# Performance work log

Hardware: AMD Instinct MI355X
Metric: run time of the kernel (lower is better)

The kernel has to match this reference:

```python
import jax, jax.numpy as jnp
import numpy as np

# Hard-coded problem constants from WENONetwork.forward()
SIGMA = 0.3
RATE = 0.1
STRIKE = 50.0
T_FINAL = 1.0
XL, XR = -6.0, 1.5
M = 80                      # spatial cells -> M+1 nodes
H = (XR - XL) / M
# explicit-Euler diffusion CFL: dt = 0.4*h^2/sigma^2
N_STEPS = int(np.ceil(T_FINAL / (0.4 * H * H / SIGMA ** 2)))
DT = T_FINAL / N_STEPS
ADV = RATE - 0.5 * SIGMA ** 2   # drift in log-price variable


def setup_inputs() -> dict:
    key = jax.random.key(0)
    k5, k6 = jax.random.split(key)
    # learned WENO weights: convex combinations over 3 candidate stencils
    omegas5 = jax.nn.softmax(jax.random.normal(k5, (M, 3), dtype=jnp.float32), axis=-1)
    omegas6 = jax.nn.softmax(jax.random.normal(k6, (M - 1, 3), dtype=jnp.float32), axis=-1)
    return {"omegas5": omegas5, "omegas6": omegas6}


def _bs_weno(omegas5, omegas6):
    # log-price grid and terminal-payoff initial condition for a call
    x = jnp.linspace(XL, XR, M + 1)
    S = STRIKE * jnp.exp(x)
    u0 = jnp.maximum(S - STRIKE, 0.0).astype(jnp.float32)

    w5_0, w5_1, w5_2 = omegas5[:, 0], omegas5[:, 1], omegas5[:, 2]  # per-interface, [M]
    w6_0, w6_1, w6_2 = omegas6[:, 0], omegas6[:, 1], omegas6[:, 2]  # per interior node, [M-1]
    s_right = S[-1]

    def step(carry, _):
        u, t = carry
        # ghost cells: flat-extend left (payoff is 0 there), linear-extrapolate right
        left = jnp.full((2,), u[0], u.dtype)
        right = u[-1] + jnp.arange(1, 3, dtype=u.dtype) * (u[-1] - u[-2])
        up = jnp.concatenate([left, u, right])  # nodes -2 .. M+2, node k -> up[k+2]

        # ---- WENO5 left-biased reconstruction at interfaces j+1/2, j = 0..M-1 ----
        um2 = up[0:M]; um1 = up[1:M + 1]; uc = up[2:M + 2]
        up1 = up[3:M + 3]; up2 = up[4:M + 4]
        f0 = (2.0 * um2 - 7.0 * um1 + 11.0 * uc) / 6.0
        f1 = (-um1 + 5.0 * uc + 2.0 * up1) / 6.0
        f2 = (2.0 * uc + 5.0 * up1 - up2) / 6.0
        uhat = w5_0 * f0 + w5_1 * f1 + w5_2 * f2          # [M] interface values
        ux = (uhat[1:] - uhat[:-1]) / H                   # [M-1] first derivative at nodes 1..M-1

        # ---- WENO-weighted second derivative at interior nodes i = 1..M-1 ----
        dm2 = up[1:M]; dm1 = up[2:M + 1]; dc = up[3:M + 2]
        dp1 = up[4:M + 3]; dp2 = up[5:M + 4]
        c0 = dm2 - 2.0 * dm1 + dc
        c1 = dm1 - 2.0 * dc + dp1
        c2 = dc - 2.0 * dp1 + dp2
        uxx = (w6_0 * c0 + w6_1 * c1 + w6_2 * c2) / (H * H)  # [M-1]

        # explicit Euler update of Black-Scholes PDE in log variable
        du = 0.5 * SIGMA ** 2 * uxx + ADV * ux - RATE * u[1:M]
        tn = t + DT
        bc_right = (s_right - STRIKE * jnp.exp(-RATE * tn)).astype(u.dtype)
        un = jnp.concatenate([jnp.zeros((1,), u.dtype),
                              u[1:M] + DT * du,
                              bc_right[None]])
        return (un, tn), None

    (uT, _), _ = jax.lax.scan(step, (u0, jnp.float32(0.0)), None, length=N_STEPS)
    return uT


def reference(omegas5, omegas6):
    return _bs_weno(omegas5, omegas6)
```

## Files before the change

### kernel.cpp

```cpp
#include <hip/hip_runtime.h>
#include <hip/hip_bf16.h>


#define MM 80
#define NSTEPS 26

__global__ __launch_bounds__(128)
void weno_bs_kernel(const float* __restrict__ om5,
                    const float* __restrict__ om6,
                    float* __restrict__ out)
{
    const float H      = 7.5f / 80.0f;
    const float DT     = 1.0f / 26.0f;
    const float SIG2H2 = 0.045f / (H * H);
    const float ADV    = 0.055f;
    const float RATE   = 0.1f;
    const float STRIKE = 50.0f;

    __shared__ float up[MM + 5];
    __shared__ float uhat[MM];

    const int i = threadIdx.x;

    float w50 = 0.f, w51 = 0.f, w52 = 0.f;
    float w60 = 0.f, w61 = 0.f, w62 = 0.f;
    if (i < MM) {
        w50 = om5[3 * i + 0];
        w51 = om5[3 * i + 1];
        w52 = om5[3 * i + 2];
    }
    if (i >= 1 && i <= MM - 1) {
        const int j = i - 1;
        w60 = om6[3 * j + 0];
        w61 = om6[3 * j + 1];
        w62 = om6[3 * j + 2];
    }

    if (i <= MM) {
        float x = -6.0f + (float)i * H;
        float S = STRIKE * expf(x);
        up[2 + i] = fmaxf(S - STRIKE, 0.0f);
    }
    const float s_right = STRIKE * expf(1.5f);
    float t = 0.0f;
    __syncthreads();

    for (int step = 0; step < NSTEPS; ++step) {
        if (i == 0) {
            float u0v = up[2];
            up[0] = u0v;
            up[1] = u0v;
            float d = up[2 + MM] - up[1 + MM];
            up[3 + MM] = up[2 + MM] + d;
            up[4 + MM] = up[2 + MM] + 2.0f * d;
        }
        __syncthreads();

        float a0 = 0.f, a1 = 0.f, a2 = 0.f, a3 = 0.f, a4 = 0.f;
        float uxx = 0.f, uold = 0.f;
        if (i < MM) {
            a0 = up[i];     a1 = up[i + 1]; a2 = up[i + 2];
            a3 = up[i + 3]; a4 = up[i + 4];
            float f0 = (2.0f * a0 - 7.0f * a1 + 11.0f * a2) * (1.0f / 6.0f);
            float f1 = (-a1 + 5.0f * a2 + 2.0f * a3) * (1.0f / 6.0f);
            float f2 = (2.0f * a2 + 5.0f * a3 - a4) * (1.0f / 6.0f);
            uhat[i] = w50 * f0 + w51 * f1 + w52 * f2;
        }
        if (i >= 1 && i <= MM - 1) {
            float c0 = a0 - 2.0f * a1 + a2;
            float c1 = a1 - 2.0f * a2 + a3;
            float c2 = a2 - 2.0f * a3 + a4;
            uxx  = w60 * c0 + w61 * c1 + w62 * c2;
            uold = a2;
        }
        t += DT;
        __syncthreads();

        if (i >= 1 && i <= MM - 1) {
            float ux = (uhat[i] - uhat[i - 1]) / H;
            float du = SIG2H2 * uxx + ADV * ux - RATE * uold;
            up[2 + i] = uold + DT * du;
        } else if (i == 0) {
            up[2] = 0.0f;
        } else if (i == MM) {
            up[2 + MM] = s_right - STRIKE * expf(-RATE * t);
        }
        __syncthreads();
    }

    if (i <= MM) {
        out[i] = up[2 + i];
    }
}

extern "C" void kernel_launch(void* const* d_in, const int* in_sizes, int n_in,
                              void* d_out, int out_size, void* d_ws, size_t ws_size,
                              hipStream_t stream) {
    const float* om5 = (const float*)d_in[0];
    const float* om6 = (const float*)d_in[1];
    float* out = (float*)d_out;
    weno_bs_kernel<<<dim3(1), dim3(128), 0, stream>>>(om5, om6, out);
}
```

Before: 66.55 us.

## Run WENO stepper in a single wavefront with register shuffles instead of LDS barriers

Replaces the 128-thread block with one 64-lane wavefront in which each lane owns two grid nodes. Neighbour values are exchanged through warp shuffles rather than shared memory, which removes all __syncthreads barriers and LDS round-trips from the 26-step serial loop. The boundary discount factor is now updated by repeated multiplication instead of an exp per step, which may differ slightly in rounding from the reference. Correctness depends on the per-lane boundary handling for lanes 0, 39 and 40.

```diff
diff --git a/kernel.cpp b/kernel.cpp
--- a/kernel.cpp
+++ b/kernel.cpp
@@ -1,96 +1,80 @@
 #include <hip/hip_runtime.h>
-#include <hip/hip_bf16.h>
 
 
 #define MM 80
 #define NSTEPS 26
 
-__global__ __launch_bounds__(128)
+__global__ __launch_bounds__(64)
 void weno_bs_kernel(const float* __restrict__ om5,
                     const float* __restrict__ om6,
                     float* __restrict__ out)
 {
-    const float H      = 7.5f / 80.0f;
+    const float H      = 0.09375f;
+    const float INV_H  = 1.0f / 0.09375f;
     const float DT     = 1.0f / 26.0f;
-    const float SIG2H2 = 0.045f / (H * H);
+    const float SIG2H2 = 0.045f / (0.09375f * 0.09375f);
     const float ADV    = 0.055f;
     const float RATE   = 0.1f;
     const float STRIKE = 50.0f;
+    const float SIXTH  = 1.0f / 6.0f;
 
-    __shared__ float up[MM + 5];
-    __shared__ float uhat[MM];
+    const int l  = threadIdx.x;
+    const int p0 = 2 * l;
+    const int p1 = 2 * l + 1;
 
-    const int i = threadIdx.x;
+    float w5a0=0.f, w5a1=0.f, w5a2=0.f, w5b0=0.f, w5b1=0.f, w5b2=0.f;
+    if (p0 < MM) { w5a0 = om5[3*p0+0]; w5a1 = om5[3*p0+1]; w5a2 = om5[3*p0+2]; }
+    if (p1 < MM) { w5b0 = om5[3*p1+0]; w5b1 = om5[3*p1+1]; w5b2 = om5[3*p1+2]; }
+    float w6a0=0.f, w6a1=0.f, w6a2=0.f, w6b0=0.f, w6b1=0.f, w6b2=0.f;
+    if (p0 >= 1 && p0 <= MM-1) { int r = 3*(p0-1); w6a0=om6[r]; w6a1=om6[r+1]; w6a2=om6[r+2]; }
+    if (p1 >= 1 && p1 <= MM-1) { int r = 3*(p1-1); w6b0=om6[r]; w6b1=om6[r+1]; w6b2=om6[r+2]; }
 
-    float w50 = 0.f, w51 = 0.f, w52 = 0.f;
-    float w60 = 0.f, w61 = 0.f, w62 = 0.f;
-    if (i < MM) {
-        w50 = om5[3 * i + 0];
-        w51 = om5[3 * i + 1];
-        w52 = om5[3 * i + 2];
-    }
-    if (i >= 1 && i <= MM - 1) {
-        const int j = i - 1;
-        w60 = om6[3 * j + 0];
-        w61 = om6[3 * j + 1];
-        w62 = om6[3 * j + 2];
+    float u0 = 0.f, u1 = 0.f;
+    if (p0 <= MM) u0 = fmaxf(STRIKE * expf(-6.0f + (float)p0 * H) - STRIKE, 0.0f);
+    if (p1 <  MM) u1 = fmaxf(STRIKE * expf(-6.0f + (float)p1 * H) - STRIKE, 0.0f);
+
+    const float s_right = STRIKE * expf(1.5f);
+    const float F = expf(-RATE * DT);
+    float e = STRIKE;
+
+    for (int s = 0; s < NSTEPS; ++s) {
+        float pm0 = __shfl_up(u0, 1);
+        float pm1 = __shfl_up(u1, 1);
+        float pp0 = __shfl_down(u0, 1);
+        float pp1 = __shfl_down(u1, 1);
+        if (l == 0)  { pm0 = u0; pm1 = u0; }
+        if (l == 39) { pp1 = 2.0f * pp0 - u1; }
+
+        float f0a = (2.0f*pm0 - 7.0f*pm1 + 11.0f*u0) * SIXTH;
+        float f1a = (-pm1 + 5.0f*u0 + 2.0f*u1) * SIXTH;
+        float f2a = (2.0f*u0 + 5.0f*u1 - pp0) * SIXTH;
+        float uh0 = w5a0*f0a + w5a1*f1a + w5a2*f2a;
+
+        float f0b = (2.0f*pm1 - 7.0f*u0 + 11.0f*u1) * SIXTH;
+        float f1b = (-u0 + 5.0f*u1 + 2.0f*pp0) * SIXTH;
+        float f2b = (2.0f*u1 + 5.0f*pp0 - pp1) * SIXTH;
+        float uh1 = w5b0*f0b + w5b1*f1b + w5b2*f2b;
+
+        float c0a = pm0 - 2.0f*pm1 + u0;
+        float c1a = pm1 - 2.0f*u0  + u1;
+        float c2a = u0  - 2.0f*u1  + pp0;
+        float c2b = u1  - 2.0f*pp0 + pp1;
+        float uxx0 = w6a0*c0a + w6a1*c1a + w6a2*c2a;
+        float uxx1 = w6b0*c1a + w6b1*c2a + w6b2*c2b;
+
+        float uhm = __shfl_up(uh1, 1);
+
+        float nu0 = u0 + DT*(SIG2H2*uxx0 + ADV*((uh0 - uhm)*INV_H) - RATE*u0);
+        float nu1 = u1 + DT*(SIG2H2*uxx1 + ADV*((uh1 - uh0)*INV_H) - RATE*u1);
+
+        e *= F;
+        if (l >= 1 && l <= 39) u0 = nu0;
+        if (l <= 39)           u1 = nu1;
+        if (l == 40)           u0 = s_right - e;
     }
 
-    if (i <= MM) {
-        float x = -6.0f + (float)i * H;
-        float S = STRIKE * expf(x);
-        up[2 + i] = fmaxf(S - STRIKE, 0.0f);
-    }
-    const float s_right = STRIKE * expf(1.5f);
-    float t = 0.0f;
-    __syncthreads();
-
-    for (int step = 0; step < NSTEPS; ++step) {
-        if (i == 0) {
-            float u0v = up[2];
-            up[0] = u0v;
-            up[1] = u0v;
-            float d = up[2 + MM] - up[1 + MM];
-            up[3 + MM] = up[2 + MM] + d;
-            up[4 + MM] = up[2 + MM] + 2.0f * d;
-        }
-        __syncthreads();
-
-        float a0 = 0.f, a1 = 0.f, a2 = 0.f, a3 = 0.f, a4 = 0.f;
-        float uxx = 0.f, uold = 0.f;
-        if (i < MM) {
-            a0 = up[i];     a1 = up[i + 1]; a2 = up[i + 2];
-            a3 = up[i + 3]; a4 = up[i + 4];
-            float f0 = (2.0f * a0 - 7.0f * a1 + 11.0f * a2) * (1.0f / 6.0f);
-            float f1 = (-a1 + 5.0f * a2 + 2.0f * a3) * (1.0f / 6.0f);
-            float f2 = (2.0f * a2 + 5.0f * a3 - a4) * (1.0f / 6.0f);
-            uhat[i] = w50 * f0 + w51 * f1 + w52 * f2;
-        }
-        if (i >= 1 && i <= MM - 1) {
-            float c0 = a0 - 2.0f * a1 + a2;
-            float c1 = a1 - 2.0f * a2 + a3;
-            float c2 = a2 - 2.0f * a3 + a4;
-            uxx  = w60 * c0 + w61 * c1 + w62 * c2;
-            uold = a2;
-        }
-        t += DT;
-        __syncthreads();
-
-        if (i >= 1 && i <= MM - 1) {
-            float ux = (uhat[i] - uhat[i - 1]) / H;
-            float du = SIG2H2 * uxx + ADV * ux - RATE * uold;
-            up[2 + i] = uold + DT * du;
-        } else if (i == 0) {
-            up[2] = 0.0f;
-        } else if (i == MM) {
-            up[2 + MM] = s_right - STRIKE * expf(-RATE * t);
-        }
-        __syncthreads();
-    }
-
-    if (i <= MM) {
-        out[i] = up[2 + i];
-    }
+    if (p0 <= MM) out[p0] = u0;
+    if (p1 <= MM) out[p1] = u1;
 }
 
 extern "C" void kernel_launch(void* const* d_in, const int* in_sizes, int n_in,
@@ -99,5 +83,5 @@
     const float* om5 = (const float*)d_in[0];
     const float* om6 = (const float*)d_in[1];
     float* out = (float*)d_out;
-    weno_bs_kernel<<<dim3(1), dim3(128), 0, stream>>>(om5, om6, out);
+    weno_bs_kernel<<<dim3(1), dim3(64), 0, stream>>>(om5, om6, out);
 }
```

Measured after the change: 60.95 us. 1.09x faster.
